# Performance work log

Measured on AMD Instinct MI355X. Metric: run time of the kernel, lower is better.

The kernel has to match this reference:

```python
import jax, jax.numpy as jnp
import numpy as np

N = 50000
E = 800000
D_IN, D_H1, D_H2, D_OUT = 128, 128, 64, 32


def setup_inputs() -> dict:
    key = jax.random.key(0)
    ks = jax.random.split(key, 8)
    x = jax.random.normal(ks[0], (N, D_IN), dtype=jnp.float32)
    edge_index = jax.random.randint(ks[1], (2, E), 0, N, dtype=jnp.int64)
    # Glorot-ish init for GCNConv weights, zero bias (PyG default bias init is zeros)
    def glorot(k, fi, fo):
        lim = np.sqrt(6.0 / (fi + fo)).astype(np.float32)
        return jax.random.uniform(k, (fi, fo), dtype=jnp.float32, minval=-lim, maxval=lim)
    return {
        "x": x,
        "edge_index": edge_index,
        "W1": glorot(ks[2], D_IN, D_H1), "b1": jnp.zeros((D_H1,), jnp.float32),
        "W2": glorot(ks[3], D_H1, D_H2), "b2": jnp.zeros((D_H2,), jnp.float32),
        "W3": glorot(ks[4], D_H2, D_OUT), "b3": jnp.zeros((D_OUT,), jnp.float32),
    }


def _gcn_norm(edge_index, n):
    # add self-loops, then symmetric normalization D^{-1/2} (A+I) D^{-1/2}
    loop = jnp.arange(n, dtype=edge_index.dtype)
    src = jnp.concatenate([edge_index[0], loop])  # [E+N]
    dst = jnp.concatenate([edge_index[1], loop])
    deg = jax.ops.segment_sum(jnp.ones_like(dst, dtype=jnp.float32), dst, num_segments=n)
    dinv = jnp.where(deg > 0, jax.lax.rsqrt(jnp.maximum(deg, 1.0)), 0.0)
    norm = dinv[src] * dinv[dst]  # [E+N]
    return src, dst, norm


def _gcn_layer(x, W, b, src, dst, norm, n):
    h = x @ W                                   # [N, d_out]
    msg = h[src] * norm[:, None]                # gather + scale, [E+N, d_out]
    agg = jax.ops.segment_sum(msg, dst, num_segments=n)
    return agg + b


def reference(x, edge_index, W1, b1, W2, b2, W3, b3):
    n = x.shape[0]
    src, dst, norm = _gcn_norm(edge_index, n)   # cached=True: computed once
    h = jax.nn.relu(_gcn_layer(x, W1, b1, src, dst, norm, n))
    h = jax.nn.relu(_gcn_layer(h, W2, b2, src, dst, norm, n))
    return _gcn_layer(h, W3, b3, src, dst, norm, n)
```

## Files before the change

### kernel.cpp

```cpp
#include <hip/hip_runtime.h>
#include <hip/hip_bf16.h>
#include <cstdint>

using short8 = __attribute__((ext_vector_type(8))) short;
using f32x4  = __attribute__((ext_vector_type(4))) float;

constexpr int CAP = 8192;

__device__ __forceinline__ unsigned f2bf_bits(float f) {
    unsigned u = __float_as_uint(f);
    return (u + 0x7fffu + ((u >> 16) & 1u)) >> 16;
}
__device__ __forceinline__ float bf_lo(unsigned u) { return __uint_as_float(u << 16); }
__device__ __forceinline__ float bf_hi(unsigned u) { return __uint_as_float(u & 0xffff0000u); }


__device__ __forceinline__ void prepack_one(const float* __restrict__ W,
                                            short* __restrict__ Wh, short* __restrict__ Wl,
                                            int DOUT, int idx) {
    int lane = idx & 63, tile = idx >> 6;
    int NT = DOUT / 16;
    int kk = tile / NT, ct = tile - kk * NT;
    int g = lane >> 4, cl = lane & 15;
    int c = ct * 16 + cl;
    short8 h8, l8;
#pragma unroll
    for (int j = 0; j < 8; ++j) {
        float w = W[(size_t)(kk * 32 + g * 8 + j) * DOUT + c];
        unsigned hb = f2bf_bits(w);
        unsigned lb = f2bf_bits(w - bf_lo(hb));
        h8[j] = (short)hb; l8[j] = (short)lb;
    }
    *reinterpret_cast<short8*>(&Wh[(size_t)idx * 8]) = h8;
    *reinterpret_cast<short8*>(&Wl[(size_t)idx * 8]) = l8;
}

__global__ __launch_bounds__(256) void prepack_all_kernel(const float* __restrict__ W1,
                                                          const float* __restrict__ W2,
                                                          const float* __restrict__ W3,
                                                          short* __restrict__ w1h, short* __restrict__ w1l,
                                                          short* __restrict__ w2h, short* __restrict__ w2l,
                                                          short* __restrict__ w3h, short* __restrict__ w3l,
                                                          int* __restrict__ bkt_cursor) {
    int idx = blockIdx.x * 256 + threadIdx.x;
    if (idx < 2048)      prepack_one(W1, w1h, w1l, 128, idx);
    else if (idx < 3072) prepack_one(W2, w2h, w2l, 64,  idx - 2048);
    else if (idx < 3328) prepack_one(W3, w3h, w3l, 32,  idx - 3072);
    else if (idx < 3584) bkt_cursor[idx - 3328] = 0;
}


__global__ __launch_bounds__(256) void bin_kernel(const int* __restrict__ src,
                                                  const int* __restrict__ dst, int E,
                                                  int* __restrict__ bkt_cursor,
                                                  unsigned* __restrict__ bin, int n) {
    __shared__ int qcnt[256];
    __shared__ int qofs[256];
    __shared__ int gbase[256];
    __shared__ uint2 staging[4096];
    const int t = threadIdx.x;
    const int e0 = blockIdx.x * 4096;
    qcnt[t] = 0;
    __syncthreads();

    int sa[16], da[16], slot[16];
#pragma unroll
    for (int k = 0; k < 16; ++k) {
        int e = e0 + k * 256 + t;
        sa[k] = -1; da[k] = 0; slot[k] = 0;
        if (e < E) {
            int ss = src[e], dd = dst[e];
            if (ss >= 0 && ss < n && dd >= 0 && dd < n) {
                sa[k] = ss; da[k] = dd;
                slot[k] = atomicAdd(&qcnt[dd >> 8], 1);
            }
        }
    }
    __syncthreads();

    qofs[t] = qcnt[t];
    __syncthreads();
    for (int off = 1; off < 256; off <<= 1) {
        int val = (t >= off) ? qofs[t - off] : 0;
        __syncthreads();
        qofs[t] += val;
        __syncthreads();
    }
    const int tot = qofs[255];
    const int myc = qcnt[t];
    if (myc > 0) gbase[t] = atomicAdd(&bkt_cursor[t], myc);
    __syncthreads();
    qofs[t] -= qcnt[t];
    __syncthreads();

#pragma unroll
    for (int k = 0; k < 16; ++k) {
        if (sa[k] >= 0)
            staging[qofs[da[k] >> 8] + slot[k]] = make_uint2((unsigned)sa[k], (unsigned)da[k]);
    }
    __syncthreads();

    for (int i = t; i < tot; i += 256) {
        uint2 en = staging[i];
        int b = (int)(en.y >> 8);
        int pos = gbase[b] + (i - qofs[b]);
        if (pos < CAP)
            bin[(size_t)b * CAP + pos] = ((en.y & 255u) << 24) | en.x;
    }
}

__global__ __launch_bounds__(256) void bucket_offsets_fill_kernel(const unsigned* __restrict__ bin,
                                                                  const int* __restrict__ bkt_cursor,
                                                                  int2* __restrict__ off2,
                                                                  float* __restrict__ dinv,
                                                                  int* __restrict__ csr, int n) {
    __shared__ int cnt[256];
    __shared__ int sh[256];
    __shared__ int cur[256];
    const int t = threadIdx.x;
    const int b = blockIdx.x;
    const int S = b * CAP;
    const int count = min(bkt_cursor[b], CAP);
    cnt[t] = 0;
    __syncthreads();
    for (int i = t; i < count; i += 256) atomicAdd(&cnt[bin[S + i] >> 24], 1);
    __syncthreads();
    const int c = cnt[t];
    sh[t] = c;
    __syncthreads();
    for (int off = 1; off < 256; off <<= 1) {
        int val = (t >= off) ? sh[t - off] : 0;
        __syncthreads();
        sh[t] += val;
        __syncthreads();
    }
    const int start = S + sh[t] - c;
    cur[t] = start;
    const int node = b * 256 + t;
    if (node < n) {
        off2[node] = make_int2(start, start + c);
        dinv[node] = rsqrtf((float)(c + 1));
    }
    __syncthreads();
    for (int i = t; i < count; i += 256) {
        unsigned p = bin[S + i];
        int pos = atomicAdd(&cur[p >> 24], 1);
        csr[pos] = (int)(p & 0xFFFFFFu);
    }
}


template<int DIN, int DOUT>
__global__ __launch_bounds__(512) void mfma_gemm_kernel(const float* __restrict__ X,
                                                        const short8* __restrict__ Wp_hi,
                                                        const short8* __restrict__ Wp_lo,
                                                        const float* __restrict__ dinv,
                                                        unsigned* __restrict__ G, int n) {
    constexpr int NT  = DOUT / 16;
    constexpr int NTW = NT / 2;
    constexpr int NK  = DIN / 32;
    constexpr int WPR = DIN / 2;
    __shared__ unsigned Xh[64 * WPR];
    __shared__ unsigned Xl[64 * WPR];
    const int t = threadIdx.x;
    const int row0 = blockIdx.x * 64;

    for (int i = t * 4; i < 64 * DIN; i += 2048) {
        int r = i / DIN, c = i % DIN;
        float4 v = make_float4(0.f, 0.f, 0.f, 0.f);
        if (row0 + r < n) v = *reinterpret_cast<const float4*>(&X[(size_t)(row0 + r) * DIN + c]);
        unsigned h0 = f2bf_bits(v.x), h1 = f2bf_bits(v.y), h2 = f2bf_bits(v.z), h3 = f2bf_bits(v.w);
        unsigned l0 = f2bf_bits(v.x - bf_lo(h0)), l1 = f2bf_bits(v.y - bf_lo(h1));
        unsigned l2 = f2bf_bits(v.z - bf_lo(h2)), l3 = f2bf_bits(v.w - bf_lo(h3));
        int w = (r * WPR + c / 2) ^ ((r & 7) << 2);
        *reinterpret_cast<uint2*>(&Xh[w]) = make_uint2(h0 | (h1 << 16), h2 | (h3 << 16));
        *reinterpret_cast<uint2*>(&Xl[w]) = make_uint2(l0 | (l1 << 16), l2 | (l3 << 16));
    }
    __syncthreads();

    const int lane = t & 63, wid = t >> 6;
    const int strip = wid >> 1, half = wid & 1;
    const int g = lane >> 4, cl = lane & 15;
    const int lrow = strip * 16 + cl;
    f32x4 acc[NTW];
#pragma unroll
    for (int i = 0; i < NTW; ++i) acc[i] = (f32x4){0.f, 0.f, 0.f, 0.f};

#pragma unroll
    for (int kk = 0; kk < NK; ++kk) {
        int wb = (lrow * WPR + kk * 16 + g * 4) ^ ((lrow & 7) << 2);
        short8 xh = *reinterpret_cast<const short8*>(&Xh[wb]);
        short8 xl = *reinterpret_cast<const short8*>(&Xl[wb]);
#pragma unroll
        for (int i = 0; i < NTW; ++i) {
            int ct = half * NTW + i;
            short8 wh = Wp_hi[(kk * NT + ct) * 64 + lane];
            short8 wl = Wp_lo[(kk * NT + ct) * 64 + lane];
            acc[i] = __builtin_amdgcn_mfma_f32_16x16x32_bf16(wh, xh, acc[i], 0, 0, 0);
            acc[i] = __builtin_amdgcn_mfma_f32_16x16x32_bf16(wh, xl, acc[i], 0, 0, 0);
            acc[i] = __builtin_amdgcn_mfma_f32_16x16x32_bf16(wl, xh, acc[i], 0, 0, 0);
        }
    }

    const int r = row0 + lrow;
    if (r < n) {
        const float s = dinv[r];
#pragma unroll
        for (int i = 0; i < NTW; ++i) {
            int c0 = (half * NTW + i) * 16 + g * 4;
            unsigned p0 = f2bf_bits(acc[i][0] * s) | (f2bf_bits(acc[i][1] * s) << 16);
            unsigned p1 = f2bf_bits(acc[i][2] * s) | (f2bf_bits(acc[i][3] * s) << 16);
            *reinterpret_cast<uint2*>(&G[(size_t)r * (DOUT / 2) + c0 / 2]) = make_uint2(p0, p1);
        }
    }
}


template<int DIN, int DOUT>
__global__ __launch_bounds__(512) void fused_agg_gemm_kernel(const unsigned* __restrict__ Gin,
                                                             const int2* __restrict__ off2,
                                                             const int* __restrict__ csr,
                                                             const float* __restrict__ dinv,
                                                             const float* __restrict__ bias,
                                                             const short8* __restrict__ Wp_hi,
                                                             const short8* __restrict__ Wp_lo,
                                                             unsigned* __restrict__ Gout, int n) {
    constexpr int NT    = DOUT / 16;
    constexpr int NTW   = NT / 2;
    constexpr int NK    = DIN / 32;
    constexpr int WPR   = DIN / 2;
    constexpr int W4    = DIN / 8;
    constexpr int LPN   = W4;
    constexpr int SLOTS = 512 / LPN;
    constexpr int ROUNDS = 64 / SLOTS;
    __shared__ unsigned Xh[64 * WPR];
    __shared__ unsigned Xl[64 * WPR];
    const int t = threadIdx.x;
    const int node0 = blockIdx.x * 64;
    const int slot = t / LPN, cw = t % LPN;
    const uint4* gB = reinterpret_cast<const uint4*>(Gin) + cw;
    const int col = cw * 8;
    const float4 bs0 = *reinterpret_cast<const float4*>(&bias[col]);
    const float4 bs1 = *reinterpret_cast<const float4*>(&bias[col + 4]);

#pragma unroll
    for (int rd = 0; rd < ROUNDS; ++rd) {
        const int r = rd * SLOTS + slot;
        const int v = node0 + r;
        unsigned hw[4] = {0u, 0u, 0u, 0u}, lw[4] = {0u, 0u, 0u, 0u};
        if (v < n) {
            float a[8], b[8];
            uint4 us = gB[(size_t)v * W4];
            a[0] = bf_lo(us.x); a[1] = bf_hi(us.x); a[2] = bf_lo(us.y); a[3] = bf_hi(us.y);
            a[4] = bf_lo(us.z); a[5] = bf_hi(us.z); a[6] = bf_lo(us.w); a[7] = bf_hi(us.w);
#pragma unroll
            for (int q = 0; q < 8; ++q) b[q] = 0.f;
            const int2 se = off2[v];
            int j = se.x;
            for (; j + 2 <= se.y; j += 2) {
                uint4 u0 = gB[(size_t)csr[j]     * W4];
                uint4 u1 = gB[(size_t)csr[j + 1] * W4];
                a[0] += bf_lo(u0.x); a[1] += bf_hi(u0.x); a[2] += bf_lo(u0.y); a[3] += bf_hi(u0.y);
                a[4] += bf_lo(u0.z); a[5] += bf_hi(u0.z); a[6] += bf_lo(u0.w); a[7] += bf_hi(u0.w);
                b[0] += bf_lo(u1.x); b[1] += bf_hi(u1.x); b[2] += bf_lo(u1.y); b[3] += bf_hi(u1.y);
                b[4] += bf_lo(u1.z); b[5] += bf_hi(u1.z); b[6] += bf_lo(u1.w); b[7] += bf_hi(u1.w);
            }
            if (j < se.y) {
                uint4 u0 = gB[(size_t)csr[j] * W4];
                a[0] += bf_lo(u0.x); a[1] += bf_hi(u0.x); a[2] += bf_lo(u0.y); a[3] += bf_hi(u0.y);
                a[4] += bf_lo(u0.z); a[5] += bf_hi(u0.z); a[6] += bf_lo(u0.w); a[7] += bf_hi(u0.w);
            }
            const float dv = dinv[v];
            const float bb[8] = {bs0.x, bs0.y, bs0.z, bs0.w, bs1.x, bs1.y, bs1.z, bs1.w};
#pragma unroll
            for (int q = 0; q < 8; ++q) {
                float o = fmaxf(dv * (a[q] + b[q]) + bb[q], 0.f);
                unsigned hb = f2bf_bits(o);
                unsigned lb = f2bf_bits(o - bf_lo(hb));
                hw[q >> 1] |= (q & 1) ? (hb << 16) : hb;
                lw[q >> 1] |= (q & 1) ? (lb << 16) : lb;
            }
        }
        const int w0 = (r * WPR + cw * 4) ^ ((r & 7) << 2);
        *reinterpret_cast<uint4*>(&Xh[w0]) = make_uint4(hw[0], hw[1], hw[2], hw[3]);
        *reinterpret_cast<uint4*>(&Xl[w0]) = make_uint4(lw[0], lw[1], lw[2], lw[3]);
    }
    __syncthreads();

    const int lane = t & 63, wid = t >> 6;
    const int strip = wid >> 1, half = wid & 1;
    const int g = lane >> 4, cl = lane & 15;
    const int lrow = strip * 16 + cl;
    f32x4 acc[NTW];
#pragma unroll
    for (int i = 0; i < NTW; ++i) acc[i] = (f32x4){0.f, 0.f, 0.f, 0.f};

#pragma unroll
    for (int kk = 0; kk < NK; ++kk) {
        int wb = (lrow * WPR + kk * 16 + g * 4) ^ ((lrow & 7) << 2);
        short8 xh = *reinterpret_cast<const short8*>(&Xh[wb]);
        short8 xl = *reinterpret_cast<const short8*>(&Xl[wb]);
#pragma unroll
        for (int i = 0; i < NTW; ++i) {
            int ct = half * NTW + i;
            short8 wh = Wp_hi[(kk * NT + ct) * 64 + lane];
            short8 wl = Wp_lo[(kk * NT + ct) * 64 + lane];
            acc[i] = __builtin_amdgcn_mfma_f32_16x16x32_bf16(wh, xh, acc[i], 0, 0, 0);
            acc[i] = __builtin_amdgcn_mfma_f32_16x16x32_bf16(wh, xl, acc[i], 0, 0, 0);
            acc[i] = __builtin_amdgcn_mfma_f32_16x16x32_bf16(wl, xh, acc[i], 0, 0, 0);
        }
    }

    const int r = node0 + lrow;
    if (r < n) {
        const float s = dinv[r];
#pragma unroll
        for (int i = 0; i < NTW; ++i) {
            int c0 = (half * NTW + i) * 16 + g * 4;
            unsigned p0 = f2bf_bits(acc[i][0] * s) | (f2bf_bits(acc[i][1] * s) << 16);
            unsigned p1 = f2bf_bits(acc[i][2] * s) | (f2bf_bits(acc[i][3] * s) << 16);
            *reinterpret_cast<uint2*>(&Gout[(size_t)r * (DOUT / 2) + c0 / 2]) = make_uint2(p0, p1);
        }
    }
}


__global__ __launch_bounds__(256) void aggregate_final_kernel(const unsigned* __restrict__ G,
                                                              const int2* __restrict__ off2,
                                                              const int* __restrict__ csr,
                                                              const float* __restrict__ dinv,
                                                              const float* __restrict__ bias,
                                                              float* __restrict__ out, int n) {
    constexpr int D = 32, W2u = 8, LPN = 8;
    const int t = threadIdx.x;
    const int v = blockIdx.x * 32 + t / LPN;
    if (v >= n) return;
    const int cw = t % LPN;
    const uint2* gB = reinterpret_cast<const uint2*>(G) + cw;

    float a[4], b[4];
    uint2 us = gB[(size_t)v * W2u];
    a[0] = bf_lo(us.x); a[1] = bf_hi(us.x); a[2] = bf_lo(us.y); a[3] = bf_hi(us.y);
#pragma unroll
    for (int q = 0; q < 4; ++q) b[q] = 0.f;

    const int2 se = off2[v];
    int j = se.x;
    for (; j + 2 <= se.y; j += 2) {
        uint2 u0 = gB[(size_t)csr[j]     * W2u];
        uint2 u1 = gB[(size_t)csr[j + 1] * W2u];
        a[0] += bf_lo(u0.x); a[1] += bf_hi(u0.x); a[2] += bf_lo(u0.y); a[3] += bf_hi(u0.y);
        b[0] += bf_lo(u1.x); b[1] += bf_hi(u1.x); b[2] += bf_lo(u1.y); b[3] += bf_hi(u1.y);
    }
    if (j < se.y) {
        uint2 u0 = gB[(size_t)csr[j] * W2u];
        a[0] += bf_lo(u0.x); a[1] += bf_hi(u0.x); a[2] += bf_lo(u0.y); a[3] += bf_hi(u0.y);
    }

    const float dv = dinv[v];
    const int col = cw * 4;
    const float4 bs = *reinterpret_cast<const float4*>(&bias[col]);
    float4 o = make_float4(dv * (a[0] + b[0]) + bs.x, dv * (a[1] + b[1]) + bs.y,
                           dv * (a[2] + b[2]) + bs.z, dv * (a[3] + b[3]) + bs.w);
    *reinterpret_cast<float4*>(&out[(size_t)v * D + col]) = o;
}


extern "C" void kernel_launch(void* const* d_in, const int* in_sizes, int n_in,
                              void* d_out, int out_size, void* d_ws, size_t ws_size,
                              hipStream_t stream) {
    const int N = 50000, E = 800000;
    const int NB  = (N + 255) / 256;
    const int NBE = (E + 4095) / 4096;
    const int NG  = (N + 63) / 64;
    const float* x  = (const float*)d_in[0];
    const int* ei = (const int*)d_in[1];
    const int* src = ei;
    const int* dst = ei + E;
    const float* W1 = (const float*)d_in[2]; const float* b1 = (const float*)d_in[3];
    const float* W2 = (const float*)d_in[4]; const float* b2 = (const float*)d_in[5];
    const float* W3 = (const float*)d_in[6]; const float* b3 = (const float*)d_in[7];
    float* out = (float*)d_out;

    char* ws = (char*)d_ws;
    size_t off = 0;
    auto alloc = [&](size_t bytes) -> void* {
        void* p = ws + off;
        off = (off + bytes + 255) & ~(size_t)255;
        return p;
    };
    int2*     off2       = (int2*)alloc((size_t)N * 8);
    float*    dinv       = (float*)alloc((size_t)N * 4);
    int*      csr        = (int*)alloc((size_t)NB * CAP * 4);
    unsigned* bin        = (unsigned*)alloc((size_t)NB * CAP * 4);
    unsigned* g1         = (unsigned*)alloc((size_t)N * 64 * 4);
    unsigned* g2         = (unsigned*)alloc((size_t)N * 32 * 4);
    unsigned* g3         = (unsigned*)alloc((size_t)N * 16 * 4);
    int*      bkt_cursor = (int*)alloc((size_t)256 * 4);
    short*    wp1h = (short*)alloc((size_t)128 * 128 * 2);
    short*    wp1l = (short*)alloc((size_t)128 * 128 * 2);
    short*    wp2h = (short*)alloc((size_t)128 * 64 * 2);
    short*    wp2l = (short*)alloc((size_t)128 * 64 * 2);
    short*    wp3h = (short*)alloc((size_t)64 * 32 * 2);
    short*    wp3l = (short*)alloc((size_t)64 * 32 * 2);
    (void)ws_size; (void)n_in; (void)in_sizes; (void)out_size;

    prepack_all_kernel<<<14, 256, 0, stream>>>(W1, W2, W3, wp1h, wp1l, wp2h, wp2l, wp3h, wp3l,
                                               bkt_cursor);
    bin_kernel<<<NBE, 256, 0, stream>>>(src, dst, E, bkt_cursor, bin, N);
    bucket_offsets_fill_kernel<<<NB, 256, 0, stream>>>(bin, bkt_cursor, off2, dinv, csr, N);

    mfma_gemm_kernel<128, 128><<<NG, 512, 0, stream>>>(x, (const short8*)wp1h, (const short8*)wp1l,
                                                       dinv, g1, N);
    fused_agg_gemm_kernel<128, 64><<<NG, 512, 0, stream>>>(g1, off2, csr, dinv, b1,
                                                           (const short8*)wp2h, (const short8*)wp2l,
                                                           g2, N);
    fused_agg_gemm_kernel<64, 32><<<NG, 512, 0, stream>>>(g2, off2, csr, dinv, b2,
                                                          (const short8*)wp3h, (const short8*)wp3l,
                                                          g3, N);
    aggregate_final_kernel<<<(N * 8 + 255) / 256, 256, 0, stream>>>(g3, off2, csr, dinv, b3, out, N);
}
```

Measured before the change: 127.6 us.

## Fuse edge binning with first GEMM and defer source-degree scaling to aggregation

The edge-binning kernel and the first MFMA GEMM now run as one launch, with blocks split by index and shared memory held in a union. The first GEMM no longer needs dinv, so it stores unscaled X·W1. The layer-2 aggregation applies dinv[src] per neighbour through fmaf, which adds an extra gathered load per edge. The neighbour loops in the aggregation kernels are also unrolled from 2 to 4 to keep more loads in flight. The intent is to remove a launch and the dependency between CSR building and GEMM1 so they overlap, at the cost of extra dinv gathers and more register use.

After: 115.6 us. -9.4%, faster.

```diff
diff --git a/kernel.cpp b/kernel.cpp
--- a/kernel.cpp
+++ b/kernel.cpp
@@ -50,62 +50,130 @@
 }
 
 
-__global__ __launch_bounds__(256) void bin_kernel(const int* __restrict__ src,
-                                                  const int* __restrict__ dst, int E,
-                                                  int* __restrict__ bkt_cursor,
-                                                  unsigned* __restrict__ bin, int n) {
-    __shared__ int qcnt[256];
-    __shared__ int qofs[256];
-    __shared__ int gbase[256];
-    __shared__ uint2 staging[4096];
+struct BinSh {
+    int qcnt[256];
+    int qofs[256];
+    int gbase[256];
+    uint2 staging[4096];
+};
+struct GemmSh {
+    unsigned Xh[64 * 64];
+    unsigned Xl[64 * 64];
+};
+union SharedU { BinSh b; GemmSh g; };
+
+__global__ __launch_bounds__(512) void bin_gemm1_kernel(const int* __restrict__ src,
+                                                        const int* __restrict__ dst, int E,
+                                                        int* __restrict__ bkt_cursor,
+                                                        unsigned* __restrict__ bin,
+                                                        const float* __restrict__ X,
+                                                        const short8* __restrict__ Wp_hi,
+                                                        const short8* __restrict__ Wp_lo,
+                                                        unsigned* __restrict__ G,
+                                                        int n, int NBE) {
+    __shared__ SharedU sh;
     const int t = threadIdx.x;
-    const int e0 = blockIdx.x * 4096;
-    qcnt[t] = 0;
-    __syncthreads();
-
-    int sa[16], da[16], slot[16];
-#pragma unroll
-    for (int k = 0; k < 16; ++k) {
-        int e = e0 + k * 256 + t;
-        sa[k] = -1; da[k] = 0; slot[k] = 0;
-        if (e < E) {
-            int ss = src[e], dd = dst[e];
-            if (ss >= 0 && ss < n && dd >= 0 && dd < n) {
-                sa[k] = ss; da[k] = dd;
-                slot[k] = atomicAdd(&qcnt[dd >> 8], 1);
+
+    if ((int)blockIdx.x < NBE) {
+        const int e0 = (int)blockIdx.x * 4096;
+        if (t < 256) sh.b.qcnt[t] = 0;
+        __syncthreads();
+        int sa[8], da[8], slot[8];
+#pragma unroll
+        for (int k = 0; k < 8; ++k) {
+            int e = e0 + k * 512 + t;
+            sa[k] = -1; da[k] = 0; slot[k] = 0;
+            if (e < E) {
+                int ss = src[e], dd = dst[e];
+                if (ss >= 0 && ss < n && dd >= 0 && dd < n) {
+                    sa[k] = ss; da[k] = dd;
+                    slot[k] = atomicAdd(&sh.b.qcnt[dd >> 8], 1);
+                }
             }
         }
-    }
-    __syncthreads();
-
-    qofs[t] = qcnt[t];
-    __syncthreads();
-    for (int off = 1; off < 256; off <<= 1) {
-        int val = (t >= off) ? qofs[t - off] : 0;
-        __syncthreads();
-        qofs[t] += val;
-        __syncthreads();
-    }
-    const int tot = qofs[255];
-    const int myc = qcnt[t];
-    if (myc > 0) gbase[t] = atomicAdd(&bkt_cursor[t], myc);
-    __syncthreads();
-    qofs[t] -= qcnt[t];
-    __syncthreads();
-
-#pragma unroll
-    for (int k = 0; k < 16; ++k) {
-        if (sa[k] >= 0)
-            staging[qofs[da[k] >> 8] + slot[k]] = make_uint2((unsigned)sa[k], (unsigned)da[k]);
-    }
-    __syncthreads();
-
-    for (int i = t; i < tot; i += 256) {
-        uint2 en = staging[i];
-        int b = (int)(en.y >> 8);
-        int pos = gbase[b] + (i - qofs[b]);
-        if (pos < CAP)
-            bin[(size_t)b * CAP + pos] = ((en.y & 255u) << 24) | en.x;
+        __syncthreads();
+        if (t < 256) sh.b.qofs[t] = sh.b.qcnt[t];
+        __syncthreads();
+        for (int off = 1; off < 256; off <<= 1) {
+            int val = 0;
+            if (t < 256 && t >= off) val = sh.b.qofs[t - off];
+            __syncthreads();
+            if (t < 256) sh.b.qofs[t] += val;
+            __syncthreads();
+        }
+        if (t < 256) {
+            int myc = sh.b.qcnt[t];
+            if (myc > 0) sh.b.gbase[t] = atomicAdd(&bkt_cursor[t], myc);
+            sh.b.qofs[t] -= myc;
+        }
+        __syncthreads();
+#pragma unroll
+        for (int k = 0; k < 8; ++k) {
+            if (sa[k] >= 0)
+                sh.b.staging[sh.b.qofs[da[k] >> 8] + slot[k]] =
+                    make_uint2((unsigned)sa[k], (unsigned)da[k]);
+        }
+        __syncthreads();
+        const int tot = sh.b.qofs[255] + sh.b.qcnt[255];
+        for (int i = t; i < tot; i += 512) {
+            uint2 en = sh.b.staging[i];
+            int b = (int)(en.y >> 8);
+            int pos = sh.b.gbase[b] + (i - sh.b.qofs[b]);
+            if (pos < CAP)
+                bin[(size_t)b * CAP + pos] = ((en.y & 255u) << 24) | en.x;
+        }
+        return;
+    }
+
+    constexpr int NT = 8, NTW = 4, NK = 4, WPR = 64;
+    const int row0 = ((int)blockIdx.x - NBE) * 64;
+
+    for (int i = t * 4; i < 64 * 128; i += 2048) {
+        int r = i / 128, c = i % 128;
+        float4 v = make_float4(0.f, 0.f, 0.f, 0.f);
+        if (row0 + r < n) v = *reinterpret_cast<const float4*>(&X[(size_t)(row0 + r) * 128 + c]);
+        unsigned h0 = f2bf_bits(v.x), h1 = f2bf_bits(v.y), h2 = f2bf_bits(v.z), h3 = f2bf_bits(v.w);
+        unsigned l0 = f2bf_bits(v.x - bf_lo(h0)), l1 = f2bf_bits(v.y - bf_lo(h1));
+        unsigned l2 = f2bf_bits(v.z - bf_lo(h2)), l3 = f2bf_bits(v.w - bf_lo(h3));
+        int w = (r * WPR + c / 2) ^ ((r & 7) << 2);
+        *reinterpret_cast<uint2*>(&sh.g.Xh[w]) = make_uint2(h0 | (h1 << 16), h2 | (h3 << 16));
+        *reinterpret_cast<uint2*>(&sh.g.Xl[w]) = make_uint2(l0 | (l1 << 16), l2 | (l3 << 16));
+    }
+    __syncthreads();
+
+    const int lane = t & 63, wid = t >> 6;
+    const int strip = wid >> 1, half = wid & 1;
+    const int g = lane >> 4, cl = lane & 15;
+    const int lrow = strip * 16 + cl;
+    f32x4 acc[NTW];
+#pragma unroll
+    for (int i = 0; i < NTW; ++i) acc[i] = (f32x4){0.f, 0.f, 0.f, 0.f};
+
+#pragma unroll
+    for (int kk = 0; kk < NK; ++kk) {
+        int wb = (lrow * WPR + kk * 16 + g * 4) ^ ((lrow & 7) << 2);
+        short8 xh = *reinterpret_cast<const short8*>(&sh.g.Xh[wb]);
+        short8 xl = *reinterpret_cast<const short8*>(&sh.g.Xl[wb]);
+#pragma unroll
+        for (int i = 0; i < NTW; ++i) {
+            int ct = half * NTW + i;
+            short8 wh = Wp_hi[(kk * NT + ct) * 64 + lane];
+            short8 wl = Wp_lo[(kk * NT + ct) * 64 + lane];
+            acc[i] = __builtin_amdgcn_mfma_f32_16x16x32_bf16(wh, xh, acc[i], 0, 0, 0);
+            acc[i] = __builtin_amdgcn_mfma_f32_16x16x32_bf16(wh, xl, acc[i], 0, 0, 0);
+            acc[i] = __builtin_amdgcn_mfma_f32_16x16x32_bf16(wl, xh, acc[i], 0, 0, 0);
+        }
+    }
+
+    const int r = row0 + lrow;
+    if (r < n) {
+#pragma unroll
+        for (int i = 0; i < NTW; ++i) {
+            int c0 = (half * NTW + i) * 16 + g * 4;
+            unsigned p0 = f2bf_bits(acc[i][0]) | (f2bf_bits(acc[i][1]) << 16);
+            unsigned p1 = f2bf_bits(acc[i][2]) | (f2bf_bits(acc[i][3]) << 16);
+            *reinterpret_cast<uint2*>(&G[(size_t)r * 64 + c0 / 2]) = make_uint2(p0, p1);
+        }
     }
 }
 
@@ -150,73 +218,7 @@
 }
 
 
-template<int DIN, int DOUT>
-__global__ __launch_bounds__(512) void mfma_gemm_kernel(const float* __restrict__ X,
-                                                        const short8* __restrict__ Wp_hi,
-                                                        const short8* __restrict__ Wp_lo,
-                                                        const float* __restrict__ dinv,
-                                                        unsigned* __restrict__ G, int n) {
-    constexpr int NT  = DOUT / 16;
-    constexpr int NTW = NT / 2;
-    constexpr int NK  = DIN / 32;
-    constexpr int WPR = DIN / 2;
-    __shared__ unsigned Xh[64 * WPR];
-    __shared__ unsigned Xl[64 * WPR];
-    const int t = threadIdx.x;
-    const int row0 = blockIdx.x * 64;
-
-    for (int i = t * 4; i < 64 * DIN; i += 2048) {
-        int r = i / DIN, c = i % DIN;
-        float4 v = make_float4(0.f, 0.f, 0.f, 0.f);
-        if (row0 + r < n) v = *reinterpret_cast<const float4*>(&X[(size_t)(row0 + r) * DIN + c]);
-        unsigned h0 = f2bf_bits(v.x), h1 = f2bf_bits(v.y), h2 = f2bf_bits(v.z), h3 = f2bf_bits(v.w);
-        unsigned l0 = f2bf_bits(v.x - bf_lo(h0)), l1 = f2bf_bits(v.y - bf_lo(h1));
-        unsigned l2 = f2bf_bits(v.z - bf_lo(h2)), l3 = f2bf_bits(v.w - bf_lo(h3));
-        int w = (r * WPR + c / 2) ^ ((r & 7) << 2);
-        *reinterpret_cast<uint2*>(&Xh[w]) = make_uint2(h0 | (h1 << 16), h2 | (h3 << 16));
-        *reinterpret_cast<uint2*>(&Xl[w]) = make_uint2(l0 | (l1 << 16), l2 | (l3 << 16));
-    }
-    __syncthreads();
-
-    const int lane = t & 63, wid = t >> 6;
-    const int strip = wid >> 1, half = wid & 1;
-    const int g = lane >> 4, cl = lane & 15;
-    const int lrow = strip * 16 + cl;
-    f32x4 acc[NTW];
-#pragma unroll
-    for (int i = 0; i < NTW; ++i) acc[i] = (f32x4){0.f, 0.f, 0.f, 0.f};
-
-#pragma unroll
-    for (int kk = 0; kk < NK; ++kk) {
-        int wb = (lrow * WPR + kk * 16 + g * 4) ^ ((lrow & 7) << 2);
-        short8 xh = *reinterpret_cast<const short8*>(&Xh[wb]);
-        short8 xl = *reinterpret_cast<const short8*>(&Xl[wb]);
-#pragma unroll
-        for (int i = 0; i < NTW; ++i) {
-            int ct = half * NTW + i;
-            short8 wh = Wp_hi[(kk * NT + ct) * 64 + lane];
-            short8 wl = Wp_lo[(kk * NT + ct) * 64 + lane];
-            acc[i] = __builtin_amdgcn_mfma_f32_16x16x32_bf16(wh, xh, acc[i], 0, 0, 0);
-            acc[i] = __builtin_amdgcn_mfma_f32_16x16x32_bf16(wh, xl, acc[i], 0, 0, 0);
-            acc[i] = __builtin_amdgcn_mfma_f32_16x16x32_bf16(wl, xh, acc[i], 0, 0, 0);
-        }
-    }
-
-    const int r = row0 + lrow;
-    if (r < n) {
-        const float s = dinv[r];
-#pragma unroll
-        for (int i = 0; i < NTW; ++i) {
-            int c0 = (half * NTW + i) * 16 + g * 4;
-            unsigned p0 = f2bf_bits(acc[i][0] * s) | (f2bf_bits(acc[i][1] * s) << 16);
-            unsigned p1 = f2bf_bits(acc[i][2] * s) | (f2bf_bits(acc[i][3] * s) << 16);
-            *reinterpret_cast<uint2*>(&G[(size_t)r * (DOUT / 2) + c0 / 2]) = make_uint2(p0, p1);
-        }
-    }
-}
-
-
-template<int DIN, int DOUT>
+template<int DIN, int DOUT, bool SCALE_IN>
 __global__ __launch_bounds__(512) void fused_agg_gemm_kernel(const unsigned* __restrict__ Gin,
                                                              const int2* __restrict__ off2,
                                                              const int* __restrict__ csr,
@@ -249,28 +251,67 @@
         const int v = node0 + r;
         unsigned hw[4] = {0u, 0u, 0u, 0u}, lw[4] = {0u, 0u, 0u, 0u};
         if (v < n) {
+            const float dv = dinv[v];
             float a[8], b[8];
             uint4 us = gB[(size_t)v * W4];
-            a[0] = bf_lo(us.x); a[1] = bf_hi(us.x); a[2] = bf_lo(us.y); a[3] = bf_hi(us.y);
-            a[4] = bf_lo(us.z); a[5] = bf_hi(us.z); a[6] = bf_lo(us.w); a[7] = bf_hi(us.w);
+            const float sself = SCALE_IN ? dv : 1.f;
+            a[0] = sself * bf_lo(us.x); a[1] = sself * bf_hi(us.x);
+            a[2] = sself * bf_lo(us.y); a[3] = sself * bf_hi(us.y);
+            a[4] = sself * bf_lo(us.z); a[5] = sself * bf_hi(us.z);
+            a[6] = sself * bf_lo(us.w); a[7] = sself * bf_hi(us.w);
 #pragma unroll
             for (int q = 0; q < 8; ++q) b[q] = 0.f;
             const int2 se = off2[v];
             int j = se.x;
-            for (; j + 2 <= se.y; j += 2) {
-                uint4 u0 = gB[(size_t)csr[j]     * W4];
-                uint4 u1 = gB[(size_t)csr[j + 1] * W4];
-                a[0] += bf_lo(u0.x); a[1] += bf_hi(u0.x); a[2] += bf_lo(u0.y); a[3] += bf_hi(u0.y);
-                a[4] += bf_lo(u0.z); a[5] += bf_hi(u0.z); a[6] += bf_lo(u0.w); a[7] += bf_hi(u0.w);
-                b[0] += bf_lo(u1.x); b[1] += bf_hi(u1.x); b[2] += bf_lo(u1.y); b[3] += bf_hi(u1.y);
-                b[4] += bf_lo(u1.z); b[5] += bf_hi(u1.z); b[6] += bf_lo(u1.w); b[7] += bf_hi(u1.w);
+            for (; j + 4 <= se.y; j += 4) {
+                int u0 = csr[j], u1 = csr[j + 1], u2 = csr[j + 2], u3 = csr[j + 3];
+                uint4 x0 = gB[(size_t)u0 * W4];
+                uint4 x1 = gB[(size_t)u1 * W4];
+                uint4 x2 = gB[(size_t)u2 * W4];
+                uint4 x3 = gB[(size_t)u3 * W4];
+                if (SCALE_IN) {
+                    float w0 = dinv[u0], w1 = dinv[u1], w2 = dinv[u2], w3 = dinv[u3];
+                    a[0] = fmaf(w0, bf_lo(x0.x), a[0]); a[1] = fmaf(w0, bf_hi(x0.x), a[1]);
+                    a[2] = fmaf(w0, bf_lo(x0.y), a[2]); a[3] = fmaf(w0, bf_hi(x0.y), a[3]);
+                    a[4] = fmaf(w0, bf_lo(x0.z), a[4]); a[5] = fmaf(w0, bf_hi(x0.z), a[5]);
+                    a[6] = fmaf(w0, bf_lo(x0.w), a[6]); a[7] = fmaf(w0, bf_hi(x0.w), a[7]);
+                    b[0] = fmaf(w1, bf_lo(x1.x), b[0]); b[1] = fmaf(w1, bf_hi(x1.x), b[1]);
+                    b[2] = fmaf(w1, bf_lo(x1.y), b[2]); b[3] = fmaf(w1, bf_hi(x1.y), b[3]);
+                    b[4] = fmaf(w1, bf_lo(x1.z), b[4]); b[5] = fmaf(w1, bf_hi(x1.z), b[5]);
+                    b[6] = fmaf(w1, bf_lo(x1.w), b[6]); b[7] = fmaf(w1, bf_hi(x1.w), b[7]);
+                    a[0] = fmaf(w2, bf_lo(x2.x), a[0]); a[1] = fmaf(w2, bf_hi(x2.x), a[1]);
+                    a[2] = fmaf(w2, bf_lo(x2.y), a[2]); a[3] = fmaf(w2, bf_hi(x2.y), a[3]);
+                    a[4] = fmaf(w2, bf_lo(x2.z), a[4]); a[5] = fmaf(w2, bf_hi(x2.z), a[5]);
+                    a[6] = fmaf(w2, bf_lo(x2.w), a[6]); a[7] = fmaf(w2, bf_hi(x2.w), a[7]);
+                    b[0] = fmaf(w3, bf_lo(x3.x), b[0]); b[1] = fmaf(w3, bf_hi(x3.x), b[1]);
+                    b[2] = fmaf(w3, bf_lo(x3.y), b[2]); b[3] = fmaf(w3, bf_hi(x3.y), b[3]);
+                    b[4] = fmaf(w3, bf_lo(x3.z), b[4]); b[5] = fmaf(w3, bf_hi(x3.z), b[5]);
+                    b[6] = fmaf(w3, bf_lo(x3.w), b[6]); b[7] = fmaf(w3, bf_hi(x3.w), b[7]);
+                } else {
+                    a[0] += bf_lo(x0.x); a[1] += bf_hi(x0.x); a[2] += bf_lo(x0.y); a[3] += bf_hi(x0.y);
+                    a[4] += bf_lo(x0.z); a[5] += bf_hi(x0.z); a[6] += bf_lo(x0.w); a[7] += bf_hi(x0.w);
+                    b[0] += bf_lo(x1.x); b[1] += bf_hi(x1.x); b[2] += bf_lo(x1.y); b[3] += bf_hi(x1.y);
+                    b[4] += bf_lo(x1.z); b[5] += bf_hi(x1.z); b[6] += bf_lo(x1.w); b[7] += bf_hi(x1.w);
+                    a[0] += bf_lo(x2.x); a[1] += bf_hi(x2.x); a[2] += bf_lo(x2.y); a[3] += bf_hi(x2.y);
+                    a[4] += bf_lo(x2.z); a[5] += bf_hi(x2.z); a[6] += bf_lo(x2.w); a[7] += bf_hi(x2.w);
+                    b[0] += bf_lo(x3.x); b[1] += bf_hi(x3.x); b[2] += bf_lo(x3.y); b[3] += bf_hi(x3.y);
+                    b[4] += bf_lo(x3.z); b[5] += bf_hi(x3.z); b[6] += bf_lo(x3.w); b[7] += bf_hi(x3.w);
+                }
             }
-            if (j < se.y) {
-                uint4 u0 = gB[(size_t)csr[j] * W4];
-                a[0] += bf_lo(u0.x); a[1] += bf_hi(u0.x); a[2] += bf_lo(u0.y); a[3] += bf_hi(u0.y);
-                a[4] += bf_lo(u0.z); a[5] += bf_hi(u0.z); a[6] += bf_lo(u0.w); a[7] += bf_hi(u0.w);
+            for (; j < se.y; ++j) {
+                int u0 = csr[j];
+                uint4 x0 = gB[(size_t)u0 * W4];
+                if (SCALE_IN) {
+                    float w0 = dinv[u0];
+                    a[0] = fmaf(w0, bf_lo(x0.x), a[0]); a[1] = fmaf(w0, bf_hi(x0.x), a[1]);
+                    a[2] = fmaf(w0, bf_lo(x0.y), a[2]); a[3] = fmaf(w0, bf_hi(x0.y), a[3]);
+                    a[4] = fmaf(w0, bf_lo(x0.z), a[4]); a[5] = fmaf(w0, bf_hi(x0.z), a[5]);
+                    a[6] = fmaf(w0, bf_lo(x0.w), a[6]); a[7] = fmaf(w0, bf_hi(x0.w), a[7]);
+                } else {
+                    a[0] += bf_lo(x0.x); a[1] += bf_hi(x0.x); a[2] += bf_lo(x0.y); a[3] += bf_hi(x0.y);
+                    a[4] += bf_lo(x0.z); a[5] += bf_hi(x0.z); a[6] += bf_lo(x0.w); a[7] += bf_hi(x0.w);
+                }
             }
-            const float dv = dinv[v];
             const float bb[8] = {bs0.x, bs0.y, bs0.z, bs0.w, bs1.x, bs1.y, bs1.z, bs1.w};
 #pragma unroll
             for (int q = 0; q < 8; ++q) {
@@ -346,15 +387,19 @@
 
     const int2 se = off2[v];
     int j = se.x;
-    for (; j + 2 <= se.y; j += 2) {
-        uint2 u0 = gB[(size_t)csr[j]     * W2u];
-        uint2 u1 = gB[(size_t)csr[j + 1] * W2u];
-        a[0] += bf_lo(u0.x); a[1] += bf_hi(u0.x); a[2] += bf_lo(u0.y); a[3] += bf_hi(u0.y);
-        b[0] += bf_lo(u1.x); b[1] += bf_hi(u1.x); b[2] += bf_lo(u1.y); b[3] += bf_hi(u1.y);
-    }
-    if (j < se.y) {
-        uint2 u0 = gB[(size_t)csr[j] * W2u];
-        a[0] += bf_lo(u0.x); a[1] += bf_hi(u0.x); a[2] += bf_lo(u0.y); a[3] += bf_hi(u0.y);
+    for (; j + 4 <= se.y; j += 4) {
+        uint2 x0 = gB[(size_t)csr[j]     * W2u];
+        uint2 x1 = gB[(size_t)csr[j + 1] * W2u];
+        uint2 x2 = gB[(size_t)csr[j + 2] * W2u];
+        uint2 x3 = gB[(size_t)csr[j + 3] * W2u];
+        a[0] += bf_lo(x0.x); a[1] += bf_hi(x0.x); a[2] += bf_lo(x0.y); a[3] += bf_hi(x0.y);
+        b[0] += bf_lo(x1.x); b[1] += bf_hi(x1.x); b[2] += bf_lo(x1.y); b[3] += bf_hi(x1.y);
+        a[0] += bf_lo(x2.x); a[1] += bf_hi(x2.x); a[2] += bf_lo(x2.y); a[3] += bf_hi(x2.y);
+        b[0] += bf_lo(x3.x); b[1] += bf_hi(x3.x); b[2] += bf_lo(x3.y); b[3] += bf_hi(x3.y);
+    }
+    for (; j < se.y; ++j) {
+        uint2 x0 = gB[(size_t)csr[j] * W2u];
+        a[0] += bf_lo(x0.x); a[1] += bf_hi(x0.x); a[2] += bf_lo(x0.y); a[3] += bf_hi(x0.y);
     }
 
     const float dv = dinv[v];
@@ -407,16 +452,15 @@
 
     prepack_all_kernel<<<14, 256, 0, stream>>>(W1, W2, W3, wp1h, wp1l, wp2h, wp2l, wp3h, wp3l,
                                                bkt_cursor);
-    bin_kernel<<<NBE, 256, 0, stream>>>(src, dst, E, bkt_cursor, bin, N);
+    bin_gemm1_kernel<<<NBE + NG, 512, 0, stream>>>(src, dst, E, bkt_cursor, bin,
+                                                   x, (const short8*)wp1h, (const short8*)wp1l,
+                                                   g1, N, NBE);
     bucket_offsets_fill_kernel<<<NB, 256, 0, stream>>>(bin, bkt_cursor, off2, dinv, csr, N);
-
-    mfma_gemm_kernel<128, 128><<<NG, 512, 0, stream>>>(x, (const short8*)wp1h, (const short8*)wp1l,
-                                                       dinv, g1, N);
-    fused_agg_gemm_kernel<128, 64><<<NG, 512, 0, stream>>>(g1, off2, csr, dinv, b1,
-                                                           (const short8*)wp2h, (const short8*)wp2l,
-                                                           g2, N);
-    fused_agg_gemm_kernel<64, 32><<<NG, 512, 0, stream>>>(g2, off2, csr, dinv, b2,
-                                                          (const short8*)wp3h, (const short8*)wp3l,
-                                                          g3, N);
+    fused_agg_gemm_kernel<128, 64, true><<<NG, 512, 0, stream>>>(g1, off2, csr, dinv, b1,
+                                                                 (const short8*)wp2h,
+                                                                 (const short8*)wp2l, g2, N);
+    fused_agg_gemm_kernel<64, 32, false><<<NG, 512, 0, stream>>>(g2, off2, csr, dinv, b2,
+                                                                 (const short8*)wp3h,
+                                                                 (const short8*)wp3l, g3, N);
     aggregate_final_kernel<<<(N * 8 + 255) / 256, 256, 0, stream>>>(g3, off2, csr, dinv, b3, out, N);
 }
```
